# Kernel tuning notes

Measured on AMD Instinct MI355X. Metric: run time of the kernel, lower is better.

Reference implementation:

```python
import jax, jax.numpy as jnp
import numpy as np
import math

N_HEADS = 16
KV_HEADS = 4
HEAD_DIM = 128
ROPE_BASE = 1000000.0


def _make_rope(seq_len, dim, base=ROPE_BASE):
    inv_freq = 1.0 / (base ** (np.arange(0, dim, 2, dtype=np.float32) / dim))
    t = np.arange(seq_len, dtype=np.float32)
    freqs = np.outer(t, inv_freq)                     # [S, dim/2]
    emb = np.concatenate([freqs, freqs], axis=-1)     # [S, dim]
    return jnp.asarray(np.cos(emb)), jnp.asarray(np.sin(emb))


def setup_inputs() -> dict:
    key = jax.random.key(0)
    ks = jax.random.split(key, 6)
    B, S, H = 2, 2048, 2048
    kv_dim = KV_HEADS * HEAD_DIM
    s = 1.0 / math.sqrt(H)
    x = jax.random.normal(ks[0], (B, S, H), jnp.float32)
    wq = jax.random.normal(ks[1], (H, H), jnp.float32) * s
    wk = jax.random.normal(ks[2], (kv_dim, H), jnp.float32) * s
    wv = jax.random.normal(ks[3], (kv_dim, H), jnp.float32) * s
    wo = jax.random.normal(ks[4], (H, H), jnp.float32) * s
    bq = jnp.zeros((H,), jnp.float32)
    bk = jnp.zeros((kv_dim,), jnp.float32)
    bv = jnp.zeros((kv_dim,), jnp.float32)
    bo = jnp.zeros((H,), jnp.float32)
    cos, sin = _make_rope(S, HEAD_DIM)
    return {"x": x, "wq": wq, "bq": bq, "wk": wk, "bk": bk,
            "wv": wv, "bv": bv, "wo": wo, "bo": bo, "cos": cos, "sin": sin}


def _rotate_half(t):
    half = t.shape[-1] // 2
    return jnp.concatenate([-t[..., half:], t[..., :half]], axis=-1)


def reference(x, wq, bq, wk, bk, wv, bv, wo, bo, cos, sin):
    B, S, H = x.shape
    hd, nh, kvh = HEAD_DIM, N_HEADS, KV_HEADS
    rep = nh // kvh

    q = (x @ wq.T + bq).reshape(B, S, nh, hd)
    k = (x @ wk.T + bk).reshape(B, S, kvh, hd)
    v = (x @ wv.T + bv).reshape(B, S, kvh, hd)

    # RoPE (rotate-half), cos/sin: [S, hd] -> broadcast over batch and heads
    c = cos[None, :, None, :]
    s_ = sin[None, :, None, :]
    q = q * c + _rotate_half(q) * s_
    k = k * c + _rotate_half(k) * s_

    # GQA: expand KV heads by rep
    k = jnp.repeat(k, rep, axis=2)   # [B, S, nh, hd]
    v = jnp.repeat(v, rep, axis=2)

    q = q.transpose(0, 2, 1, 3)      # [B, nh, S, hd]
    k = k.transpose(0, 2, 1, 3)
    v = v.transpose(0, 2, 1, 3)

    score = jnp.einsum('bhqd,bhkd->bhqk', q, k) / math.sqrt(hd)
    causal = jnp.triu(jnp.full((S, S), -jnp.inf, jnp.float32), k=1)
    score = score + causal
    attn = jax.nn.softmax(score.astype(jnp.float32), axis=-1).astype(q.dtype)

    out = jnp.einsum('bhqk,bhkd->bhqd', attn, v)   # [B, nh, S, hd]
    out = out.transpose(0, 2, 1, 3).reshape(B, S, nh * hd)
    return out @ wo.T + bo
```

## Files before the change

kernel.cpp:

```cpp
#include <hip/hip_runtime.h>

typedef unsigned short u16;
typedef __bf16 bf16x8 __attribute__((ext_vector_type(8)));
typedef float  f32x4  __attribute__((ext_vector_type(4)));

#define SEQ 2048

__device__ __forceinline__ float bf2f(u16 u) {
    union { unsigned int i; float f; } c;
    c.i = ((unsigned int)u) << 16;
    return c.f;
}
__device__ __forceinline__ u16 f2bf(float f) {
    union { float f; unsigned int i; } c;
    c.f = f;
    unsigned int u = c.i;
    u += 0x7FFFu + ((u >> 16) & 1u);
    return (u16)(u >> 16);
}

__device__ __forceinline__ void gl_lds16(const u16* g, u16* l) {
    __builtin_amdgcn_global_load_lds(
        (const __attribute__((address_space(1))) unsigned int*)(g),
        (__attribute__((address_space(3))) unsigned int*)(l), 16, 0, 0);
}

__device__ __forceinline__ void cvt4(const float* s, u16* d) {
    float4 v = *(const float4*)s;
    ushort4 o;
    o.x = f2bf(v.x); o.y = f2bf(v.y); o.z = f2bf(v.z); o.w = f2bf(v.w);
    *(ushort4*)d = o;
}

__global__ void prep(const float* __restrict__ x,
                     const float* __restrict__ wq, const float* __restrict__ wk,
                     const float* __restrict__ wv,
                     const float* __restrict__ bq, const float* __restrict__ bk,
                     const float* __restrict__ bv,
                     u16* __restrict__ xb, u16* __restrict__ wqkvb,
                     float* __restrict__ biasb)
{
    const int E0 = 2097152;
    const int E1 = E0 + 1048576;
    const int E2 = E1 + 262144;
    const int E3 = E2 + 262144;
    const int E4 = E3 + 768;
    int i = blockIdx.x * blockDim.x + threadIdx.x;
    int stride = gridDim.x * blockDim.x;
    for (; i < E4; i += stride) {
        if (i < E0)      cvt4(x  + (size_t)i * 4,        xb    + (size_t)i * 4);
        else if (i < E1) cvt4(wq + (size_t)(i - E0) * 4, wqkvb + (size_t)(i - E0) * 4);
        else if (i < E2) cvt4(wk + (size_t)(i - E1) * 4, wqkvb + 4194304 + (size_t)(i - E1) * 4);
        else if (i < E3) cvt4(wv + (size_t)(i - E2) * 4, wqkvb + 5242880 + (size_t)(i - E2) * 4);
        else {
            int j = i - E3;
            const float* src = (j < 512) ? (bq + j * 4)
                             : (j < 640) ? (bk + (j - 512) * 4)
                                         : (bv + (j - 640) * 4);
            *(float4*)&biasb[j * 4] = *(const float4*)src;
        }
    }
}

__global__ void cvt_f32_bf16(const float* __restrict__ in, u16* __restrict__ out, int n4) {
    int i = blockIdx.x * blockDim.x + threadIdx.x;
    int stride = gridDim.x * blockDim.x;
    for (; i < n4; i += stride) cvt4(in + (size_t)i * 4, out + (size_t)i * 4);
}

template<int MODE>
__global__ __launch_bounds__(256) void gemm_bt(
    const u16* __restrict__ A, const u16* __restrict__ B,
    const float* __restrict__ bias, float* __restrict__ C,
    u16* __restrict__ qb, u16* __restrict__ kb, u16* __restrict__ vt,
    int M, int N, int K)
{
    __shared__ __align__(16) u16 lA[128 * 32];
    __shared__ __align__(16) u16 lB[128 * 32];
    const int tid   = threadIdx.x;
    const int lane  = tid & 63;
    const int wave  = tid >> 6;
    const int waveM = (wave >> 1) * 64;
    const int waveN = (wave & 1) * 64;
    const int bm = blockIdx.x * 128;
    const int bn = blockIdx.y * 128;
    const int lrow = lane & 15;
    const int koff = (lane >> 4) * 8;

    f32x4 acc[4][4] = {};

    for (int k0 = 0; k0 < K; k0 += 32) {
        __syncthreads();
#pragma unroll
        for (int p = 0; p < 2; ++p) {
            int idx = p * 256 + tid;
            int row = idx >> 2;
            int ch  = idx & 3;
            gl_lds16(&A[(size_t)(bm + row) * K + k0 + ch * 8], &lA[(p * 256 + wave * 64) * 8]);
            gl_lds16(&B[(size_t)(bn + row) * K + k0 + ch * 8], &lB[(p * 256 + wave * 64) * 8]);
        }
        __syncthreads();

        bf16x8 af[4], bfr[4];
#pragma unroll
        for (int i = 0; i < 4; ++i)
            af[i] = *(const bf16x8*)&lA[(waveM + i * 16 + lrow) * 32 + koff];
#pragma unroll
        for (int j = 0; j < 4; ++j)
            bfr[j] = *(const bf16x8*)&lB[(waveN + j * 16 + lrow) * 32 + koff];
#pragma unroll
        for (int i = 0; i < 4; ++i)
#pragma unroll
            for (int j = 0; j < 4; ++j)
                acc[i][j] = __builtin_amdgcn_mfma_f32_16x16x32_bf16(
                    af[i], bfr[j], acc[i][j], 0, 0, 0);
    }

    const int r4 = (lane >> 4) * 4;
    const int cn = lane & 15;
#pragma unroll
    for (int i = 0; i < 4; ++i) {
#pragma unroll
        for (int j = 0; j < 4; ++j) {
            int row0 = bm + waveM + i * 16 + r4;
            int col  = bn + waveN + j * 16 + cn;
            float bc = bias[col];
#pragma unroll
            for (int r = 0; r < 4; ++r) {
                float val = acc[i][j][r] + bc;
                if (MODE == 0) {
                    C[(size_t)(row0 + r) * N + col] = val;
                } else {
                    int row = row0 + r;
                    int b = row >> 11;
                    int s = row & 2047;
                    int d = col & 127;
                    u16 o = f2bf(val);
                    if (col < 2048) {
                        int h = col >> 7;
                        qb[(((size_t)(b * 16 + h) * SEQ) + s) * 128 + d] = o;
                    } else if (col < 2560) {
                        int h = (col - 2048) >> 7;
                        kb[(((size_t)(b * 4 + h) * SEQ) + s) * 128 + d] = o;
                    } else {
                        int h = (col - 2560) >> 7;
                        vt[(((size_t)(b * 4 + h) * 128) + d) * SEQ + s] = o;
                    }
                }
            }
        }
    }
}

__global__ void rope_inplace(u16* __restrict__ qb, u16* __restrict__ kb,
                             const float* __restrict__ cosb, const float* __restrict__ sinb)
{
    const int n = (65536 + 16384) * 64;
    int i = blockIdx.x * blockDim.x + threadIdx.x;
    if (i >= n) return;
    int d0  = i & 63;
    int row = i >> 6;
    u16* base;
    if (row < 65536) base = qb + (size_t)row * 128;
    else             base = kb + (size_t)(row - 65536) * 128;
    int s = row & (SEQ - 1);
    float c  = cosb[s * 128 + d0];
    float sn = sinb[s * 128 + d0];
    float a0 = bf2f(base[d0]);
    float a1 = bf2f(base[d0 + 64]);
    base[d0]      = f2bf(a0 * c - a1 * sn);
    base[d0 + 64] = f2bf(a1 * c + a0 * sn);
}

__global__ __launch_bounds__(256, 2) void attn_mfma(
    const u16* __restrict__ qb, const u16* __restrict__ kb,
    const u16* __restrict__ vt, u16* __restrict__ ob)
{
    __shared__ __align__(16) u16 Ks[2][4][64][32];
    __shared__ __align__(16) u16 Vts[2][2][128][32];
    __shared__ __align__(16) u16 Ph[4][16][64];

    const int id   = blockIdx.x;
    const int s8   = id & 7;
    const int n    = id >> 3;
    const int pair = n & 15;
    const int h_lo = n >> 4;
    const int b    = s8 >> 2;
    const int kvh  = s8 & 3;
    const int h    = kvh * 4 + h_lo;
    const int qA   = pair, qB = 31 - pair;

    const int tid  = threadIdx.x;
    const int lane = tid & 63;
    const int w    = tid >> 6;
    const int c16  = lane & 15;
    const int quad = lane >> 4;
    const int T    = w >> 1;
    const int sub  = w & 1;
    const int qT   = T ? qB : qA;
    const float qscale = 0.08838834764831845f * 1.4426950408889634f;

    const u16* kbase  = kb + ((size_t)(b * 4 + kvh) * SEQ) * 128;
    const u16* vtbase = vt + ((size_t)(b * 4 + kvh) * 128) * 128 * (SEQ / 128);

    bf16x8 qf[2][4];
#pragma unroll
    for (int s = 0; s < 2; ++s) {
        const u16* qp = qb + (((size_t)(b * 16 + h)) * SEQ + qT * 64 + sub * 32 + s * 16 + c16) * 128;
#pragma unroll
        for (int kk = 0; kk < 4; ++kk) {
            bf16x8 t = *(const bf16x8*)(qp + kk * 32 + quad * 8);
#pragma unroll
            for (int e = 0; e < 8; ++e) t[e] = (__bf16)((float)t[e] * qscale);
            qf[s][kk] = t;
        }
    }

    int ksrc[4], vsrc[4];
#pragma unroll
    for (int it = 0; it < 4; ++it) {
        int o  = (it * 4 + w) * 1024 + lane * 16;
        int kk = o >> 12;
        int r  = (o >> 6) & 63;
        int c  = (o >> 4) & 3;
        ksrc[it] = r * 128 + kk * 32 + c * 8;
        int p2 = o >> 13;
        int d  = (o >> 6) & 127;
        vsrc[it] = d * SEQ + p2 * 32 + c * 8;
    }

    const int nB = qB + 1;
    const int rowL0 = qT * 64 + sub * 32 + quad * 4;

    f32x4 o[2][8] = {};
    float l[2][4] = {};

    u16* KsF  = &Ks[0][0][0][0];
    u16* VtsF = &Vts[0][0][0][0];

#pragma unroll
    for (int it = 0; it < 4; ++it) {
        gl_lds16(kbase  + ksrc[it], KsF  + (it * 4 + w) * 512);
        gl_lds16(vtbase + vsrc[it], VtsF + (it * 4 + w) * 512);
    }
    __syncthreads();

    for (int kt = 0; kt < nB; ++kt) {
        const int cur = kt & 1;

        if (kt + 1 < nB) {
            const u16* kg = kbase  + (size_t)(kt + 1) * (64 * 128);
            const u16* vg = vtbase + (kt + 1) * 64;
            u16* kd = KsF  + ((kt + 1) & 1) * (4 * 64 * 32);
            u16* vd = VtsF + ((kt + 1) & 1) * (2 * 128 * 32);
#pragma unroll
            for (int it = 0; it < 4; ++it) {
                gl_lds16(kg + ksrc[it], kd + (it * 4 + w) * 512);
                gl_lds16(vg + vsrc[it], vd + (it * 4 + w) * 512);
            }
        }

        if (T == 1 || kt <= qA) {
            f32x4 sS[2][4] = {};
#pragma unroll
            for (int kk = 0; kk < 4; ++kk)
#pragma unroll
                for (int j = 0; j < 4; ++j) {
                    bf16x8 kf = *(const bf16x8*)&Ks[cur][kk][j * 16 + c16][quad * 8];
                    sS[0][j] = __builtin_amdgcn_mfma_f32_16x16x32_bf16(qf[0][kk], kf, sS[0][j], 0, 0, 0);
                    sS[1][j] = __builtin_amdgcn_mfma_f32_16x16x32_bf16(qf[1][kk], kf, sS[1][j], 0, 0, 0);
                }

            if (kt == qT) {
#pragma unroll
                for (int s = 0; s < 2; ++s)
#pragma unroll
                    for (int j = 0; j < 4; ++j)
#pragma unroll
                        for (int rr = 0; rr < 4; ++rr)
                            if (kt * 64 + j * 16 + c16 > rowL0 + s * 16 + rr) sS[s][j][rr] = -1e30f;
            }

            bf16x8 pa[2][2];
#pragma unroll
            for (int s = 0; s < 2; ++s) {
#pragma unroll
                for (int jj = 0; jj < 4; ++jj)
#pragma unroll
                    for (int rr = 0; rr < 4; ++rr) {
                        float p = __builtin_amdgcn_exp2f(sS[s][jj][rr]);
                        l[s][rr] += p;
                        int row = quad * 4 + rr;
                        *(__bf16*)&Ph[w][row][(((jj * 2 + (c16 >> 3)) + row) & 7) * 8 + (c16 & 7)] = (__bf16)p;
                    }
#pragma unroll
                for (int k2 = 0; k2 < 2; ++k2)
                    pa[s][k2] = *(const bf16x8*)&Ph[w][c16][(((k2 * 4 + quad) + c16) & 7) * 8];
            }

#pragma unroll
            for (int k2 = 0; k2 < 2; ++k2)
#pragma unroll
                for (int nt = 0; nt < 8; ++nt) {
                    bf16x8 vf = *(const bf16x8*)&Vts[cur][k2][nt * 16 + c16][quad * 8];
                    o[0][nt] = __builtin_amdgcn_mfma_f32_16x16x32_bf16(pa[0][k2], vf, o[0][nt], 0, 0, 0);
                    o[1][nt] = __builtin_amdgcn_mfma_f32_16x16x32_bf16(pa[1][k2], vf, o[1][nt], 0, 0, 0);
                }
        }

        __syncthreads();
    }

#pragma unroll
    for (int s = 0; s < 2; ++s) {
        float li[4];
#pragma unroll
        for (int rr = 0; rr < 4; ++rr) {
            float la = l[s][rr];
            la += __shfl_xor(la, 1);
            la += __shfl_xor(la, 2);
            la += __shfl_xor(la, 4);
            la += __shfl_xor(la, 8);
            li[rr] = 1.0f / la;
        }
        const size_t rowG = (size_t)b * SEQ + rowL0 + s * 16;
#pragma unroll
        for (int nt = 0; nt < 8; ++nt)
#pragma unroll
            for (int rr = 0; rr < 4; ++rr)
                ob[(rowG + rr) * 2048 + h * 128 + nt * 16 + c16] = f2bf(o[s][nt][rr] * li[rr]);
    }
}

extern "C" void kernel_launch(void* const* d_in, const int* in_sizes, int n_in,
                              void* d_out, int out_size, void* d_ws, size_t ws_size,
                              hipStream_t stream) {
    const float* x    = (const float*)d_in[0];
    const float* wq   = (const float*)d_in[1];
    const float* bq   = (const float*)d_in[2];
    const float* wk   = (const float*)d_in[3];
    const float* bk   = (const float*)d_in[4];
    const float* wv   = (const float*)d_in[5];
    const float* bv   = (const float*)d_in[6];
    const float* wo   = (const float*)d_in[7];
    const float* bo   = (const float*)d_in[8];
    const float* cosb = (const float*)d_in[9];
    const float* sinb = (const float*)d_in[10];
    float* out = (float*)d_out;

    char* ws = (char*)d_ws;
    const size_t OFF_WQKV = 0;
    const size_t OFF_BIAS = 12582912;
    const size_t OFF_QB   = 12599296;
    const size_t OFF_KB   = 29376512;
    const size_t OFF_VT   = 33570816;
    const size_t OFF_XB   = 37765120;

    u16*   wqkvb = (u16*)(ws + OFF_WQKV);
    u16*   wob   = (u16*)(ws + OFF_WQKV);
    float* biasb = (float*)(ws + OFF_BIAS);
    u16*   qb2   = (u16*)(ws + OFF_QB);
    u16*   kb2   = (u16*)(ws + OFF_KB);
    u16*   vt2   = (u16*)(ws + OFF_VT);
    u16*   xb    = (u16*)(ws + OFF_XB);
    u16*   attnb = (u16*)(ws + OFF_XB);

    prep<<<4096, 256, 0, stream>>>(x, wq, wk, wv, bq, bk, bv, xb, wqkvb, biasb);

    gemm_bt<1><<<dim3(32, 24), 256, 0, stream>>>(xb, wqkvb, biasb, nullptr,
                                                 qb2, kb2, vt2, 4096, 3072, 2048);

    cvt_f32_bf16<<<4096, 256, 0, stream>>>(wo, wob, 1048576);

    rope_inplace<<<((65536 + 16384) * 64) / 256, 256, 0, stream>>>(qb2, kb2, cosb, sinb);

    attn_mfma<<<512, 256, 0, stream>>>(qb2, kb2, vt2, attnb);

    gemm_bt<0><<<dim3(32, 16), 256, 0, stream>>>(attnb, wob, bo, out,
                                                 nullptr, nullptr, nullptr, 4096, 2048, 2048);
}
```

Baseline: 347.2 us.

## Use 256x256-tile 512-thread double-buffered GEMM for fused QKV projection

Adds a new gemm256 kernel with 256x256 block tiles, 8 waves, XOR-swizzled LDS staging via global_load_lds, two-stage double buffering and setprio around MFMA bursts, and uses it for the QKV projection instead of the 128-tile gemm_bt. The larger tiles raise arithmetic intensity and cut global/LDS traffic per flop. The grid shrinks to 192 blocks, which may underfill the 256 CUs, and LDS use is high. The vtbase expression change in attention is algebraically identical.

Result: slower. 361.3 us (+4.1%).

```diff
diff --git a/kernel.cpp b/kernel.cpp
--- a/kernel.cpp
+++ b/kernel.cpp
@@ -152,6 +152,160 @@
     }
 }
 
+template<int MODE>
+__global__ __launch_bounds__(512, 2) void gemm256(
+    const u16* __restrict__ A, const u16* __restrict__ B,
+    const float* __restrict__ bias, float* __restrict__ C,
+    u16* __restrict__ qb, u16* __restrict__ kb, u16* __restrict__ vt,
+    int M, int N, int K)
+{
+    __shared__ __align__(16) u16 L[2][2][256 * 64];
+
+    const int tid  = threadIdx.x;
+    const int lane = tid & 63;
+    const int w    = tid >> 6;
+    const int wm   = w >> 2;
+    const int wn   = w & 3;
+    const int lrow = lane & 15;
+    const int quad = lane >> 4;
+
+    const int bm = blockIdx.x * 256;
+    const int bn = blockIdx.y * 256;
+
+    int srow[4], soff[4];
+#pragma unroll
+    for (int i = 0; i < 4; ++i) {
+        int Lc  = i * 512 + tid;
+        int row = Lc >> 3;
+        soff[i] = ((Lc & 7) ^ (row & 7)) * 8;
+        srow[i] = row;
+    }
+    const u16* Ag = A + (size_t)bm * K;
+    const u16* Bg = B + (size_t)bn * K;
+
+    f32x4 acc[8][4] = {};
+    const int NT = K >> 6;
+
+#pragma unroll
+    for (int i = 0; i < 4; ++i) {
+        gl_lds16(Ag + (size_t)srow[i] * K + soff[i],      &L[0][0][(i * 512 + w * 64) * 8]);
+        gl_lds16(Bg + (size_t)srow[i] * K + soff[i],      &L[0][1][(i * 512 + w * 64) * 8]);
+    }
+#pragma unroll
+    for (int i = 0; i < 4; ++i) {
+        gl_lds16(Ag + (size_t)srow[i] * K + 64 + soff[i], &L[1][0][(i * 512 + w * 64) * 8]);
+        gl_lds16(Bg + (size_t)srow[i] * K + 64 + soff[i], &L[1][1][(i * 512 + w * 64) * 8]);
+    }
+    asm volatile("s_waitcnt vmcnt(8)" ::: "memory");
+    __builtin_amdgcn_s_barrier();
+
+    int cur = 0;
+    for (int kt = 0; kt < NT; ++kt) {
+        const u16* At = &L[cur][0][0];
+        const u16* Bt = &L[cur][1][0];
+
+        bf16x8 bF[2][4], aF[2][4];
+#pragma unroll
+        for (int kk = 0; kk < 2; ++kk)
+#pragma unroll
+            for (int j = 0; j < 4; ++j) {
+                int row = wn * 64 + j * 16 + lrow;
+                bF[kk][j] = *(const bf16x8*)&Bt[row * 64 + (((kk * 4 + quad) ^ (lrow & 7)) * 8)];
+            }
+#pragma unroll
+        for (int kk = 0; kk < 2; ++kk)
+#pragma unroll
+            for (int i = 0; i < 4; ++i) {
+                int row = wm * 128 + i * 16 + lrow;
+                aF[kk][i] = *(const bf16x8*)&At[row * 64 + (((kk * 4 + quad) ^ (lrow & 7)) * 8)];
+            }
+        asm volatile("s_waitcnt lgkmcnt(0)" ::: "memory");
+        __builtin_amdgcn_sched_barrier(0);
+        __builtin_amdgcn_s_setprio(1);
+#pragma unroll
+        for (int kk = 0; kk < 2; ++kk)
+#pragma unroll
+            for (int i = 0; i < 4; ++i)
+#pragma unroll
+                for (int j = 0; j < 4; ++j)
+                    acc[i][j] = __builtin_amdgcn_mfma_f32_16x16x32_bf16(
+                        aF[kk][i], bF[kk][j], acc[i][j], 0, 0, 0);
+        __builtin_amdgcn_s_setprio(0);
+
+#pragma unroll
+        for (int kk = 0; kk < 2; ++kk)
+#pragma unroll
+            for (int i = 0; i < 4; ++i) {
+                int row = wm * 128 + 64 + i * 16 + lrow;
+                aF[kk][i] = *(const bf16x8*)&At[row * 64 + (((kk * 4 + quad) ^ (lrow & 7)) * 8)];
+            }
+        asm volatile("s_waitcnt lgkmcnt(0)" ::: "memory");
+        __builtin_amdgcn_sched_barrier(0);
+        __builtin_amdgcn_s_setprio(1);
+#pragma unroll
+        for (int kk = 0; kk < 2; ++kk)
+#pragma unroll
+            for (int i = 0; i < 4; ++i)
+#pragma unroll
+                for (int j = 0; j < 4; ++j)
+                    acc[4 + i][j] = __builtin_amdgcn_mfma_f32_16x16x32_bf16(
+                        aF[kk][i], bF[kk][j], acc[4 + i][j], 0, 0, 0);
+        __builtin_amdgcn_s_setprio(0);
+
+        __builtin_amdgcn_s_barrier();
+
+        if (kt + 2 < NT) {
+            const u16* Ag2 = Ag + (kt + 2) * 64;
+            const u16* Bg2 = Bg + (kt + 2) * 64;
+#pragma unroll
+            for (int i = 0; i < 4; ++i) {
+                gl_lds16(Ag2 + (size_t)srow[i] * K + soff[i], &L[cur][0][(i * 512 + w * 64) * 8]);
+                gl_lds16(Bg2 + (size_t)srow[i] * K + soff[i], &L[cur][1][(i * 512 + w * 64) * 8]);
+            }
+            asm volatile("s_waitcnt vmcnt(8)" ::: "memory");
+        } else {
+            asm volatile("s_waitcnt vmcnt(0)" ::: "memory");
+        }
+        __builtin_amdgcn_s_barrier();
+        cur ^= 1;
+    }
+
+    const int r4 = quad * 4;
+    const int cn = lrow;
+#pragma unroll
+    for (int i = 0; i < 8; ++i) {
+#pragma unroll
+        for (int j = 0; j < 4; ++j) {
+            int row0 = bm + wm * 128 + i * 16 + r4;
+            int col  = bn + wn * 64 + j * 16 + cn;
+            float bc = bias[col];
+#pragma unroll
+            for (int r = 0; r < 4; ++r) {
+                float val = acc[i][j][r] + bc;
+                if (MODE == 0) {
+                    C[(size_t)(row0 + r) * N + col] = val;
+                } else {
+                    int row = row0 + r;
+                    int b = row >> 11;
+                    int s = row & 2047;
+                    int d = col & 127;
+                    u16 o = f2bf(val);
+                    if (col < 2048) {
+                        int h = col >> 7;
+                        qb[(((size_t)(b * 16 + h) * SEQ) + s) * 128 + d] = o;
+                    } else if (col < 2560) {
+                        int h = (col - 2048) >> 7;
+                        kb[(((size_t)(b * 4 + h) * SEQ) + s) * 128 + d] = o;
+                    } else {
+                        int h = (col - 2560) >> 7;
+                        vt[(((size_t)(b * 4 + h) * 128) + d) * SEQ + s] = o;
+                    }
+                }
+            }
+        }
+    }
+}
+
 __global__ void rope_inplace(u16* __restrict__ qb, u16* __restrict__ kb,
                              const float* __restrict__ cosb, const float* __restrict__ sinb)
 {
@@ -201,7 +355,7 @@
     const float qscale = 0.08838834764831845f * 1.4426950408889634f;
 
     const u16* kbase  = kb + ((size_t)(b * 4 + kvh) * SEQ) * 128;
-    const u16* vtbase = vt + ((size_t)(b * 4 + kvh) * 128) * 128 * (SEQ / 128);
+    const u16* vtbase = vt + ((size_t)(b * 4 + kvh) * 128) * SEQ;
 
     bf16x8 qf[2][4];
 #pragma unroll
@@ -367,7 +521,7 @@
 
     prep<<<4096, 256, 0, stream>>>(x, wq, wk, wv, bq, bk, bv, xb, wqkvb, biasb);
 
-    gemm_bt<1><<<dim3(32, 24), 256, 0, stream>>>(xb, wqkvb, biasb, nullptr,
+    gemm256<1><<<dim3(16, 12), 512, 0, stream>>>(xb, wqkvb, biasb, nullptr,
                                                  qb2, kb2, vt2, 4096, 3072, 2048);
 
     cvt_f32_bf16<<<4096, 256, 0, stream>>>(wo, wob, 1048576);
```

## Fuse Q RoPE into attention Q load and swizzle GEMM block order

Applied to the files above, without the earlier changes.

RoPE for Q is now applied inside the attention kernel as Q fragments are loaded, so the separate in-place pass only rotates K. This removes a full read-modify-write of the Q buffer. The GEMMs now launch on a 1D grid and remap block IDs in groups of eight, which changes the order tiles are scheduled across compute units and may improve cache locality. In exchange, the attention prologue reads cos/sin from global memory per lane.

Result: no change. 351.4 us (+1.2%).

```diff
diff --git a/kernel.cpp b/kernel.cpp
--- a/kernel.cpp
+++ b/kernel.cpp
@@ -82,8 +82,14 @@
     const int wave  = tid >> 6;
     const int waveM = (wave >> 1) * 64;
     const int waveN = (wave & 1) * 64;
-    const int bm = blockIdx.x * 128;
-    const int bn = blockIdx.y * 128;
+
+    const int nwg = gridDim.x;
+    const int cpx = nwg >> 3;
+    const int idb = blockIdx.x;
+    const int swz = (idb & 7) * cpx + (idb >> 3);
+    const int bm = (swz & 31) * 128;
+    const int bn = (swz >> 5) * 128;
+
     const int lrow = lane & 15;
     const int koff = (lane >> 4) * 8;
 
@@ -152,17 +158,15 @@
     }
 }
 
-__global__ void rope_inplace(u16* __restrict__ qb, u16* __restrict__ kb,
-                             const float* __restrict__ cosb, const float* __restrict__ sinb)
+__global__ void rope_k(u16* __restrict__ kb,
+                       const float* __restrict__ cosb, const float* __restrict__ sinb)
 {
-    const int n = (65536 + 16384) * 64;
+    const int n = 16384 * 64;
     int i = blockIdx.x * blockDim.x + threadIdx.x;
     if (i >= n) return;
     int d0  = i & 63;
     int row = i >> 6;
-    u16* base;
-    if (row < 65536) base = qb + (size_t)row * 128;
-    else             base = kb + (size_t)(row - 65536) * 128;
+    u16* base = kb + (size_t)row * 128;
     int s = row & (SEQ - 1);
     float c  = cosb[s * 128 + d0];
     float sn = sinb[s * 128 + d0];
@@ -174,7 +178,8 @@
 
 __global__ __launch_bounds__(256, 2) void attn_mfma(
     const u16* __restrict__ qb, const u16* __restrict__ kb,
-    const u16* __restrict__ vt, u16* __restrict__ ob)
+    const u16* __restrict__ vt, u16* __restrict__ ob,
+    const float* __restrict__ cosb, const float* __restrict__ sinb)
 {
     __shared__ __align__(16) u16 Ks[2][4][64][32];
     __shared__ __align__(16) u16 Vts[2][2][128][32];
@@ -201,18 +206,30 @@
     const float qscale = 0.08838834764831845f * 1.4426950408889634f;
 
     const u16* kbase  = kb + ((size_t)(b * 4 + kvh) * SEQ) * 128;
-    const u16* vtbase = vt + ((size_t)(b * 4 + kvh) * 128) * 128 * (SEQ / 128);
+    const u16* vtbase = vt + ((size_t)(b * 4 + kvh) * 128) * SEQ;
 
     bf16x8 qf[2][4];
 #pragma unroll
     for (int s = 0; s < 2; ++s) {
-        const u16* qp = qb + (((size_t)(b * 16 + h)) * SEQ + qT * 64 + sub * 32 + s * 16 + c16) * 128;
-#pragma unroll
-        for (int kk = 0; kk < 4; ++kk) {
-            bf16x8 t = *(const bf16x8*)(qp + kk * 32 + quad * 8);
-#pragma unroll
-            for (int e = 0; e < 8; ++e) t[e] = (__bf16)((float)t[e] * qscale);
-            qf[s][kk] = t;
+        const int spos = qT * 64 + sub * 32 + s * 16 + c16;
+        const u16* qp = qb + (((size_t)(b * 16 + h)) * SEQ + spos) * 128;
+        bf16x8 t[4];
+#pragma unroll
+        for (int kk = 0; kk < 4; ++kk)
+            t[kk] = *(const bf16x8*)(qp + kk * 32 + quad * 8);
+#pragma unroll
+        for (int kk = 0; kk < 2; ++kk) {
+            const float* cp = cosb + (size_t)spos * 128 + kk * 32 + quad * 8;
+            const float* sp = sinb + (size_t)spos * 128 + kk * 32 + quad * 8;
+#pragma unroll
+            for (int e = 0; e < 8; ++e) {
+                float a0 = (float)t[kk][e];
+                float a1 = (float)t[kk + 2][e];
+                float c  = cp[e];
+                float sn = sp[e];
+                qf[s][kk][e]     = (__bf16)((a0 * c - a1 * sn) * qscale);
+                qf[s][kk + 2][e] = (__bf16)((a1 * c + a0 * sn) * qscale);
+            }
         }
     }
 
@@ -367,15 +384,15 @@
 
     prep<<<4096, 256, 0, stream>>>(x, wq, wk, wv, bq, bk, bv, xb, wqkvb, biasb);
 
-    gemm_bt<1><<<dim3(32, 24), 256, 0, stream>>>(xb, wqkvb, biasb, nullptr,
-                                                 qb2, kb2, vt2, 4096, 3072, 2048);
+    gemm_bt<1><<<768, 256, 0, stream>>>(xb, wqkvb, biasb, nullptr,
+                                        qb2, kb2, vt2, 4096, 3072, 2048);
 
     cvt_f32_bf16<<<4096, 256, 0, stream>>>(wo, wob, 1048576);
 
-    rope_inplace<<<((65536 + 16384) * 64) / 256, 256, 0, stream>>>(qb2, kb2, cosb, sinb);
-
-    attn_mfma<<<512, 256, 0, stream>>>(qb2, kb2, vt2, attnb);
-
-    gemm_bt<0><<<dim3(32, 16), 256, 0, stream>>>(attnb, wob, bo, out,
-                                                 nullptr, nullptr, nullptr, 4096, 2048, 2048);
-}
+    rope_k<<<4096, 256, 0, stream>>>(kb2, cosb, sinb);
+
+    attn_mfma<<<512, 256, 0, stream>>>(qb2, kb2, vt2, attnb, cosb, sinb);
+
+    gemm_bt<0><<<512, 256, 0, stream>>>(attnb, wob, bo, out,
+                                        nullptr, nullptr, nullptr, 4096, 2048, 2048);
+}
```
